# Optimization experiments

Measured on AMD Instinct MI355X. Metric: run time of the kernel, lower is better.

Reference implementation:

```python
import jax, jax.numpy as jnp
import numpy as np

H = 256        # hidden_size
MAX_LEN = 200  # position table has MAX_LEN+1 rows
B = 4096       # number of sessions


def setup_inputs() -> dict:
    rng = np.random.RandomState(0)
    # ragged session lengths in [10, 100)
    seq_len = rng.randint(10, 100, size=B).astype(np.int64)
    T = int(seq_len.sum())
    # reverse positions: len-1, ..., 1, 0 per session (as the torch code uses)
    reverse_pos = np.concatenate([np.arange(l - 1, -1, -1) for l in seq_len]).astype(np.int64)

    key = jax.random.key(0)
    ks = jax.random.split(key, 8)
    def lin(k, fin, fout):
        # torch Linear init ~ U(-1/sqrt(fin), 1/sqrt(fin)); store as [fin, fout]
        lim = 1.0 / np.sqrt(fin)
        kw, kb = jax.random.split(k)
        W = jax.random.uniform(kw, (fin, fout), jnp.float32, -lim, lim)
        b = jax.random.uniform(kb, (fout,), jnp.float32, -lim, lim)
        return W, b

    hidden = jax.random.normal(ks[0], (T, H), jnp.float32)
    pos_table = jax.random.normal(ks[1], (MAX_LEN + 1, H), jnp.float32)
    W_pos, b_pos = lin(ks[2], 2 * H, H)   # W_pos_inter
    W1, b1 = lin(ks[3], H, H)             # W_1_inter
    W2, b2 = lin(ks[4], H, H)             # W_2_inter
    qw, qb = lin(ks[5], H, 1)             # q_inter

    return {
        "hidden": hidden,
        "pos_table": pos_table,
        "W_pos": W_pos, "b_pos": b_pos,
        "W1": W1, "b1": b1,
        "W2": W2, "b2": b2,
        "qw": qw, "qb": qb,
        "seq_len": jnp.asarray(seq_len),
        "reverse_pos": jnp.asarray(reverse_pos),
    }


def reference(hidden, pos_table, W_pos, b_pos, W1, b1, W2, b2, qw, qb, seq_len, reverse_pos):
    T = hidden.shape[0]
    nb = seq_len.shape[0]
    # segment id per token (sessions are contiguous)
    seg = jnp.repeat(jnp.arange(nb), seq_len, total_repeat_length=T)  # [T]
    # per-session mean, gathered back per token (v_mean_repeat_concat)
    sess_mean = jax.ops.segment_sum(hidden, seg, num_segments=nb)
    sess_mean = sess_mean / seq_len[:, None].astype(hidden.dtype)
    v_mean = sess_mean[seg]                                           # [T, H]
    # position-augmented hidden: tanh(W_pos_inter([hidden; pos_emb]))
    pos_emb = pos_table[reverse_pos]                                  # [T, H]
    pos_hidden = jnp.tanh(jnp.concatenate([hidden, pos_emb], -1) @ W_pos + b_pos)
    # alpha = q_inter(sigmoid(W_1_inter(v_mean) + W_2_inter(pos_hidden)))
    gate = jax.nn.sigmoid(v_mean @ W1 + b1 + pos_hidden @ W2 + b2)
    alpha = gate @ qw + qb                                            # [T, 1]
    # per-session weighted sum of hidden
    h_s = jax.ops.segment_sum(alpha * hidden, seg, num_segments=nb)   # [B, H]
    return h_s
```

## Files before the change

kernel.cpp:

```cpp
#include <hip/hip_runtime.h>
#include <hip/hip_bf16.h>
#include <stdint.h>

#define HD 256
#define BM 64
#define BK 32
#define PAD 8

typedef __bf16 bf16x8 __attribute__((ext_vector_type(8)));
typedef float f32x4 __attribute__((ext_vector_type(4)));
typedef unsigned short ushort8 __attribute__((ext_vector_type(8)));

__device__ __forceinline__ unsigned short f2bf(float f) {
    unsigned int x = __float_as_uint(f);
    unsigned int r = (x + 0x7FFFu + ((x >> 16) & 1u)) >> 16;
    return (unsigned short)r;
}

__global__ void scan_kernel(const int* __restrict__ seq_len, int* __restrict__ offsets, int B) {
    __shared__ int sums[256];
    int tid = threadIdx.x;
    int per = (B + 255) / 256;
    int b0 = tid * per;
    int local[32];
    int tot = 0;
    for (int i = 0; i < per && i < 32; ++i) {
        int b = b0 + i;
        int v = (b < B) ? seq_len[b] : 0;
        local[i] = tot;
        tot += v;
    }
    sums[tid] = tot;
    __syncthreads();
    for (int off = 1; off < 256; off <<= 1) {
        int v = (tid >= off) ? sums[tid - off] : 0;
        __syncthreads();
        sums[tid] += v;
        __syncthreads();
    }
    int start = sums[tid] - tot;
    for (int i = 0; i < per && i < 32; ++i) {
        int b = b0 + i;
        if (b < B) offsets[b] = start + local[i];
    }
    if (tid == 255) offsets[B] = sums[255];
}

__global__ void seg_kernel(const int* __restrict__ offsets, int* __restrict__ seg) {
    int b = blockIdx.x;
    int s = offsets[b], e = offsets[b + 1];
    for (int t = s + threadIdx.x; t < e; t += blockDim.x) seg[t] = b;
}

__global__ void mean_kernel(const float* __restrict__ hidden, const int* __restrict__ offsets,
                            float* __restrict__ mean) {
    int b = blockIdx.x;
    int s = offsets[b], e = offsets[b + 1];
    int tid = threadIdx.x;
    int g = tid >> 6, c = tid & 63;
    float4 acc = {0.f, 0.f, 0.f, 0.f};
    for (int t = s + g; t < e; t += 4) {
        const float4 v = *reinterpret_cast<const float4*>(hidden + (size_t)t * HD + c * 4);
        acc.x += v.x; acc.y += v.y; acc.z += v.z; acc.w += v.w;
    }
    __shared__ float4 part[4][64];
    part[g][c] = acc;
    __syncthreads();
    if (g == 0) {
        float4 a0 = part[0][c], a1 = part[1][c], a2 = part[2][c], a3 = part[3][c];
        float inv = 1.0f / (float)(e - s);
        float4 m;
        m.x = (a0.x + a1.x + a2.x + a3.x) * inv;
        m.y = (a0.y + a1.y + a2.y + a3.y) * inv;
        m.z = (a0.z + a1.z + a2.z + a3.z) * inv;
        m.w = (a0.w + a1.w + a2.w + a3.w) * inv;
        *reinterpret_cast<float4*>(mean + (size_t)b * HD + c * 4) = m;
    }
}

__global__ void transpose_kernel(const float* __restrict__ Wp, const float* __restrict__ W1,
                                 const float* __restrict__ W2,
                                 unsigned short* __restrict__ WphT, unsigned short* __restrict__ WpbT,
                                 unsigned short* __restrict__ W1T, unsigned short* __restrict__ W2T) {
    int n = blockIdx.x;
    int k = threadIdx.x;
    WphT[n * HD + k] = f2bf(Wp[k * HD + n]);
    WpbT[n * HD + k] = f2bf(Wp[(HD + k) * HD + n]);
    W1T[n * HD + k]  = f2bf(W1[k * HD + n]);
    W2T[n * HD + k]  = f2bf(W2[k * HD + n]);
}

__global__ __launch_bounds__(256) void gemm_bias_kernel(
    const float* __restrict__ A, int M,
    const unsigned short* __restrict__ BT,
    const float* __restrict__ bias1, const float* __restrict__ bias2,
    float* __restrict__ out) {
    __shared__ __align__(16) unsigned short As[BM][BK + PAD];
    __shared__ __align__(16) unsigned short Bs[HD][BK + PAD];
    int tid = threadIdx.x;
    int m0 = blockIdx.x * BM;
    int wave = tid >> 6, lane = tid & 63, quad = lane >> 4, cc = lane & 15;
    int nb = wave * 64;
    f32x4 acc[4][4];
    for (int i = 0; i < 4; ++i) for (int j = 0; j < 4; ++j) acc[i][j] = (f32x4){0.f, 0.f, 0.f, 0.f};
    int arow = tid >> 2, acg = (tid & 3) * 8;

    for (int kc = 0; kc < HD; kc += BK) {
        {
            int m = m0 + arow;
            float4 f0 = {0,0,0,0}, f1 = {0,0,0,0};
            if (m < M) {
                const float4* p = reinterpret_cast<const float4*>(A + (size_t)m * HD + kc + acg);
                f0 = p[0]; f1 = p[1];
            }
            ushort8 pk;
            pk[0] = f2bf(f0.x); pk[1] = f2bf(f0.y); pk[2] = f2bf(f0.z); pk[3] = f2bf(f0.w);
            pk[4] = f2bf(f1.x); pk[5] = f2bf(f1.y); pk[6] = f2bf(f1.z); pk[7] = f2bf(f1.w);
            *reinterpret_cast<ushort8*>(&As[arow][acg]) = pk;
        }
        for (int i = 0; i < 4; ++i) {
            int n = i * 64 + (tid >> 2);
            int c8 = (tid & 3) * 8;
            ushort8 v = *reinterpret_cast<const ushort8*>(BT + (size_t)n * HD + kc + c8);
            *reinterpret_cast<ushort8*>(&Bs[n][c8]) = v;
        }
        __syncthreads();
        bf16x8 af[4], bfr[4];
        for (int mf = 0; mf < 4; ++mf) af[mf] = *reinterpret_cast<const bf16x8*>(&As[mf * 16 + cc][quad * 8]);
        for (int nf = 0; nf < 4; ++nf) bfr[nf] = *reinterpret_cast<const bf16x8*>(&Bs[nb + nf * 16 + cc][quad * 8]);
        for (int mf = 0; mf < 4; ++mf)
            for (int nf = 0; nf < 4; ++nf)
                acc[mf][nf] = __builtin_amdgcn_mfma_f32_16x16x32_bf16(af[mf], bfr[nf], acc[mf][nf], 0, 0, 0);
        __syncthreads();
    }
    for (int mf = 0; mf < 4; ++mf)
        for (int nf = 0; nf < 4; ++nf)
            for (int r = 0; r < 4; ++r) {
                int row = m0 + mf * 16 + quad * 4 + r;
                int col = nb + nf * 16 + cc;
                if (row < M) {
                    float v = acc[mf][nf][r] + bias1[col];
                    if (bias2) v += bias2[col];
                    out[(size_t)row * HD + col] = v;
                }
            }
}

__global__ __launch_bounds__(256) void main_kernel(
    const float* __restrict__ hidden, int T,
    const unsigned short* __restrict__ WphT,
    const unsigned short* __restrict__ W2T,
    const float* __restrict__ P2,
    const float* __restrict__ u,
    const float* __restrict__ qw, const float* __restrict__ qb,
    const int* __restrict__ rp, const int* __restrict__ seg,
    float* __restrict__ alpha) {
    __shared__ __align__(16) unsigned short As[BM][BK + PAD];
    __shared__ __align__(16) unsigned short Bs[HD][BK + PAD];
    __shared__ __align__(16) unsigned short Ph[BM][HD + PAD];
    __shared__ int rp_s[BM];
    __shared__ int seg_s[BM];
    __shared__ float alpha_s[BM];

    int tid = threadIdx.x;
    int t0 = blockIdx.x * BM;
    if (tid < BM) {
        int t = t0 + tid;
        rp_s[tid]  = (t < T) ? rp[t] : 0;
        seg_s[tid] = (t < T) ? seg[t] : 0;
        alpha_s[tid] = qb[0];
    }
    int wave = tid >> 6, lane = tid & 63, quad = lane >> 4, cc = lane & 15;
    int nb = wave * 64;
    f32x4 acc[4][4];
    for (int i = 0; i < 4; ++i) for (int j = 0; j < 4; ++j) acc[i][j] = (f32x4){0.f, 0.f, 0.f, 0.f};
    int arow = tid >> 2, acg = (tid & 3) * 8;

    for (int kc = 0; kc < HD; kc += BK) {
        {
            int t = t0 + arow;
            float4 f0 = {0,0,0,0}, f1 = {0,0,0,0};
            if (t < T) {
                const float4* p = reinterpret_cast<const float4*>(hidden + (size_t)t * HD + kc + acg);
                f0 = p[0]; f1 = p[1];
            }
            ushort8 pk;
            pk[0] = f2bf(f0.x); pk[1] = f2bf(f0.y); pk[2] = f2bf(f0.z); pk[3] = f2bf(f0.w);
            pk[4] = f2bf(f1.x); pk[5] = f2bf(f1.y); pk[6] = f2bf(f1.z); pk[7] = f2bf(f1.w);
            *reinterpret_cast<ushort8*>(&As[arow][acg]) = pk;
        }
        for (int i = 0; i < 4; ++i) {
            int n = i * 64 + (tid >> 2);
            int c8 = (tid & 3) * 8;
            ushort8 v = *reinterpret_cast<const ushort8*>(WphT + (size_t)n * HD + kc + c8);
            *reinterpret_cast<ushort8*>(&Bs[n][c8]) = v;
        }
        __syncthreads();
        bf16x8 af[4], bfr[4];
        for (int mf = 0; mf < 4; ++mf) af[mf] = *reinterpret_cast<const bf16x8*>(&As[mf * 16 + cc][quad * 8]);
        for (int nf = 0; nf < 4; ++nf) bfr[nf] = *reinterpret_cast<const bf16x8*>(&Bs[nb + nf * 16 + cc][quad * 8]);
        for (int mf = 0; mf < 4; ++mf)
            for (int nf = 0; nf < 4; ++nf)
                acc[mf][nf] = __builtin_amdgcn_mfma_f32_16x16x32_bf16(af[mf], bfr[nf], acc[mf][nf], 0, 0, 0);
        __syncthreads();
    }

    for (int mf = 0; mf < 4; ++mf)
        for (int nf = 0; nf < 4; ++nf)
            for (int r = 0; r < 4; ++r) {
                int row = mf * 16 + quad * 4 + r;
                int col = nb + nf * 16 + cc;
                float v = acc[mf][nf][r] + P2[(size_t)rp_s[row] * HD + col];
                Ph[row][col] = f2bf(tanhf(v));
                acc[mf][nf][r] = 0.f;
            }
    __syncthreads();

    for (int kc = 0; kc < HD; kc += BK) {
        for (int i = 0; i < 4; ++i) {
            int n = i * 64 + (tid >> 2);
            int c8 = (tid & 3) * 8;
            ushort8 v = *reinterpret_cast<const ushort8*>(W2T + (size_t)n * HD + kc + c8);
            *reinterpret_cast<ushort8*>(&Bs[n][c8]) = v;
        }
        __syncthreads();
        bf16x8 af[4], bfr[4];
        for (int mf = 0; mf < 4; ++mf) af[mf] = *reinterpret_cast<const bf16x8*>(&Ph[mf * 16 + cc][kc + quad * 8]);
        for (int nf = 0; nf < 4; ++nf) bfr[nf] = *reinterpret_cast<const bf16x8*>(&Bs[nb + nf * 16 + cc][quad * 8]);
        for (int mf = 0; mf < 4; ++mf)
            for (int nf = 0; nf < 4; ++nf)
                acc[mf][nf] = __builtin_amdgcn_mfma_f32_16x16x32_bf16(af[mf], bfr[nf], acc[mf][nf], 0, 0, 0);
        __syncthreads();
    }

    float qwv[4];
    for (int nf = 0; nf < 4; ++nf) qwv[nf] = qw[nb + nf * 16 + cc];
    for (int mf = 0; mf < 4; ++mf)
        for (int r = 0; r < 4; ++r) {
            int row = mf * 16 + quad * 4 + r;
            const float* urow = u + (size_t)seg_s[row] * HD;
            float s = 0.f;
            for (int nf = 0; nf < 4; ++nf) {
                float g = acc[mf][nf][r] + urow[nb + nf * 16 + cc];
                g = 1.0f / (1.0f + __expf(-g));
                s += g * qwv[nf];
            }
            s += __shfl_xor(s, 1);
            s += __shfl_xor(s, 2);
            s += __shfl_xor(s, 4);
            s += __shfl_xor(s, 8);
            if (cc == 0) atomicAdd(&alpha_s[row], s);
        }
    __syncthreads();
    if (tid < BM) {
        int t = t0 + tid;
        if (t < T) alpha[t] = alpha_s[tid];
    }
}

__global__ void hs_kernel(const float* __restrict__ hidden, const float* __restrict__ alpha,
                          const int* __restrict__ offsets, float* __restrict__ out) {
    int b = blockIdx.x;
    int s = offsets[b], e = offsets[b + 1];
    int tid = threadIdx.x;
    __shared__ float al[256];
    for (int i = tid; i < e - s; i += 256) al[i] = alpha[s + i];
    __syncthreads();
    int g = tid >> 6, c = tid & 63;
    float4 acc = {0.f, 0.f, 0.f, 0.f};
    for (int t = s + g; t < e; t += 4) {
        float a = al[t - s];
        const float4 v = *reinterpret_cast<const float4*>(hidden + (size_t)t * HD + c * 4);
        acc.x += a * v.x; acc.y += a * v.y; acc.z += a * v.z; acc.w += a * v.w;
    }
    __shared__ float4 part[4][64];
    part[g][c] = acc;
    __syncthreads();
    if (g == 0) {
        float4 a0 = part[0][c], a1 = part[1][c], a2 = part[2][c], a3 = part[3][c];
        float4 m;
        m.x = a0.x + a1.x + a2.x + a3.x;
        m.y = a0.y + a1.y + a2.y + a3.y;
        m.z = a0.z + a1.z + a2.z + a3.z;
        m.w = a0.w + a1.w + a2.w + a3.w;
        *reinterpret_cast<float4*>(out + (size_t)b * HD + c * 4) = m;
    }
}

extern "C" void kernel_launch(void* const* d_in, const int* in_sizes, int n_in,
                              void* d_out, int out_size, void* d_ws, size_t ws_size,
                              hipStream_t stream) {
    (void)n_in; (void)out_size; (void)ws_size;
    const float* hidden    = (const float*)d_in[0];
    const float* pos_table = (const float*)d_in[1];
    const float* W_pos     = (const float*)d_in[2];
    const float* b_pos     = (const float*)d_in[3];
    const float* W1        = (const float*)d_in[4];
    const float* b1        = (const float*)d_in[5];
    const float* W2        = (const float*)d_in[6];
    const float* b2        = (const float*)d_in[7];
    const float* qw        = (const float*)d_in[8];
    const float* qb        = (const float*)d_in[9];
    const int* seq_len     = (const int*)d_in[10];
    const int* reverse_pos = (const int*)d_in[11];

    int T  = in_sizes[0] / HD;
    int B  = in_sizes[10];
    int NP = in_sizes[1] / HD;

    char* ws = (char*)d_ws;
    auto carve = [&](size_t bytes) -> char* {
        char* p = ws;
        ws += (bytes + 255) & ~(size_t)255;
        return p;
    };
    int* offsets         = (int*)carve((size_t)(B + 1) * sizeof(int));
    int* seg             = (int*)carve((size_t)T * sizeof(int));
    float* mean          = (float*)carve((size_t)B * HD * sizeof(float));
    float* u             = (float*)carve((size_t)B * HD * sizeof(float));
    float* P2            = (float*)carve((size_t)NP * HD * sizeof(float));
    unsigned short* WphT = (unsigned short*)carve((size_t)HD * HD * 2);
    unsigned short* WpbT = (unsigned short*)carve((size_t)HD * HD * 2);
    unsigned short* W1T  = (unsigned short*)carve((size_t)HD * HD * 2);
    unsigned short* W2T  = (unsigned short*)carve((size_t)HD * HD * 2);
    float* alpha         = (float*)carve((size_t)T * sizeof(float));

    scan_kernel<<<1, 256, 0, stream>>>(seq_len, offsets, B);
    seg_kernel<<<B, 64, 0, stream>>>(offsets, seg);
    mean_kernel<<<B, 256, 0, stream>>>(hidden, offsets, mean);
    transpose_kernel<<<HD, HD, 0, stream>>>(W_pos, W1, W2, WphT, WpbT, W1T, W2T);
    gemm_bias_kernel<<<(NP + BM - 1) / BM, 256, 0, stream>>>(pos_table, NP, WpbT, b_pos, nullptr, P2);
    gemm_bias_kernel<<<(B + BM - 1) / BM, 256, 0, stream>>>(mean, B, W1T, b1, b2, u);
    main_kernel<<<(T + BM - 1) / BM, 256, 0, stream>>>(hidden, T, WphT, W2T, P2, u, qw, qb,
                                                       reverse_pos, seg, alpha);
    hs_kernel<<<B, 256, 0, stream>>>(hidden, alpha, offsets, (float*)d_out);
}
```

Measured before the change: 654.1 us.

## Stage full A tile in LDS once, read weights from global, fuse seg into mean

The GEMM kernels now load the entire 64x256 activation tile into LDS once, converted to bf16. Weight fragments are read directly from global memory (L2-resident) instead of being staged through LDS each K step, which removes the per-iteration barriers. The first GEMM in main_kernel is transposed (weights as A, tokens as B) so the tanh epilogue can write vectorized bf16 results back into the same LDS buffer, and tanhf is replaced by an exp-based formula. The seg fill is folded into mean_kernel to drop one launch, and __launch_bounds__(256,4) asks for higher occupancy, at the risk of more global weight traffic and register pressure.

```diff
diff --git a/kernel.cpp b/kernel.cpp
--- a/kernel.cpp
+++ b/kernel.cpp
@@ -5,11 +5,13 @@
 #define HD 256
 #define BM 64
 #define BK 32
-#define PAD 8
+#define APAD 8
+#define ASTRIDE (HD + APAD)
 
 typedef __bf16 bf16x8 __attribute__((ext_vector_type(8)));
 typedef float f32x4 __attribute__((ext_vector_type(4)));
-typedef unsigned short ushort8 __attribute__((ext_vector_type(8)));
+typedef unsigned short ushort8v __attribute__((ext_vector_type(8)));
+typedef unsigned short us4 __attribute__((ext_vector_type(4)));
 
 __device__ __forceinline__ unsigned short f2bf(float f) {
     unsigned int x = __float_as_uint(f);
@@ -46,17 +48,12 @@
     if (tid == 255) offsets[B] = sums[255];
 }
 
-__global__ void seg_kernel(const int* __restrict__ offsets, int* __restrict__ seg) {
+__global__ void mean_kernel(const float* __restrict__ hidden, const int* __restrict__ offsets,
+                            float* __restrict__ mean, int* __restrict__ seg) {
     int b = blockIdx.x;
     int s = offsets[b], e = offsets[b + 1];
-    for (int t = s + threadIdx.x; t < e; t += blockDim.x) seg[t] = b;
-}
-
-__global__ void mean_kernel(const float* __restrict__ hidden, const int* __restrict__ offsets,
-                            float* __restrict__ mean) {
-    int b = blockIdx.x;
-    int s = offsets[b], e = offsets[b + 1];
-    int tid = threadIdx.x;
+    int tid = threadIdx.x;
+    for (int t = s + tid; t < e; t += 256) seg[t] = b;
     int g = tid >> 6, c = tid & 63;
     float4 acc = {0.f, 0.f, 0.f, 0.f};
     for (int t = s + g; t < e; t += 4) {
@@ -95,43 +92,41 @@
     const unsigned short* __restrict__ BT,
     const float* __restrict__ bias1, const float* __restrict__ bias2,
     float* __restrict__ out) {
-    __shared__ __align__(16) unsigned short As[BM][BK + PAD];
-    __shared__ __align__(16) unsigned short Bs[HD][BK + PAD];
+    __shared__ __align__(16) unsigned short As[BM][ASTRIDE];
     int tid = threadIdx.x;
     int m0 = blockIdx.x * BM;
     int wave = tid >> 6, lane = tid & 63, quad = lane >> 4, cc = lane & 15;
     int nb = wave * 64;
     f32x4 acc[4][4];
     for (int i = 0; i < 4; ++i) for (int j = 0; j < 4; ++j) acc[i][j] = (f32x4){0.f, 0.f, 0.f, 0.f};
-    int arow = tid >> 2, acg = (tid & 3) * 8;
-
-    for (int kc = 0; kc < HD; kc += BK) {
-        {
-            int m = m0 + arow;
+
+    {
+        int row = tid >> 2;
+        int m = m0 + row;
+        for (int i = 0; i < 8; ++i) {
+            int cg = ((tid & 3) + 4 * i) * 8;
             float4 f0 = {0,0,0,0}, f1 = {0,0,0,0};
             if (m < M) {
-                const float4* p = reinterpret_cast<const float4*>(A + (size_t)m * HD + kc + acg);
+                const float4* p = reinterpret_cast<const float4*>(A + (size_t)m * HD + cg);
                 f0 = p[0]; f1 = p[1];
             }
-            ushort8 pk;
+            ushort8v pk;
             pk[0] = f2bf(f0.x); pk[1] = f2bf(f0.y); pk[2] = f2bf(f0.z); pk[3] = f2bf(f0.w);
             pk[4] = f2bf(f1.x); pk[5] = f2bf(f1.y); pk[6] = f2bf(f1.z); pk[7] = f2bf(f1.w);
-            *reinterpret_cast<ushort8*>(&As[arow][acg]) = pk;
-        }
-        for (int i = 0; i < 4; ++i) {
-            int n = i * 64 + (tid >> 2);
-            int c8 = (tid & 3) * 8;
-            ushort8 v = *reinterpret_cast<const ushort8*>(BT + (size_t)n * HD + kc + c8);
-            *reinterpret_cast<ushort8*>(&Bs[n][c8]) = v;
-        }
-        __syncthreads();
-        bf16x8 af[4], bfr[4];
-        for (int mf = 0; mf < 4; ++mf) af[mf] = *reinterpret_cast<const bf16x8*>(&As[mf * 16 + cc][quad * 8]);
-        for (int nf = 0; nf < 4; ++nf) bfr[nf] = *reinterpret_cast<const bf16x8*>(&Bs[nb + nf * 16 + cc][quad * 8]);
-        for (int mf = 0; mf < 4; ++mf)
+            *reinterpret_cast<ushort8v*>(&As[row][cg]) = pk;
+        }
+    }
+    __syncthreads();
+
+    for (int kc = 0; kc < HD; kc += BK) {
+        bf16x8 bfr[4];
+        for (int nf = 0; nf < 4; ++nf)
+            bfr[nf] = *reinterpret_cast<const bf16x8*>(BT + (size_t)(nb + nf * 16 + cc) * HD + kc + quad * 8);
+        for (int mf = 0; mf < 4; ++mf) {
+            bf16x8 af = *reinterpret_cast<const bf16x8*>(&As[mf * 16 + cc][kc + quad * 8]);
             for (int nf = 0; nf < 4; ++nf)
-                acc[mf][nf] = __builtin_amdgcn_mfma_f32_16x16x32_bf16(af[mf], bfr[nf], acc[mf][nf], 0, 0, 0);
-        __syncthreads();
+                acc[mf][nf] = __builtin_amdgcn_mfma_f32_16x16x32_bf16(af, bfr[nf], acc[mf][nf], 0, 0, 0);
+        }
     }
     for (int mf = 0; mf < 4; ++mf)
         for (int nf = 0; nf < 4; ++nf)
@@ -146,7 +141,7 @@
             }
 }
 
-__global__ __launch_bounds__(256) void main_kernel(
+__global__ __launch_bounds__(256, 4) void main_kernel(
     const float* __restrict__ hidden, int T,
     const unsigned short* __restrict__ WphT,
     const unsigned short* __restrict__ W2T,
@@ -155,93 +150,98 @@
     const float* __restrict__ qw, const float* __restrict__ qb,
     const int* __restrict__ rp, const int* __restrict__ seg,
     float* __restrict__ alpha) {
-    __shared__ __align__(16) unsigned short As[BM][BK + PAD];
-    __shared__ __align__(16) unsigned short Bs[HD][BK + PAD];
-    __shared__ __align__(16) unsigned short Ph[BM][HD + PAD];
+    __shared__ __align__(16) unsigned short Ah[BM][ASTRIDE];
     __shared__ int rp_s[BM];
     __shared__ int seg_s[BM];
     __shared__ float alpha_s[BM];
 
     int tid = threadIdx.x;
     int t0 = blockIdx.x * BM;
+    int wave = tid >> 6, lane = tid & 63, quad = lane >> 4, cc = lane & 15;
+    int mb = wave * 64;
+
+    {
+        int row = tid >> 2;
+        int t = t0 + row;
+        for (int i = 0; i < 8; ++i) {
+            int cg = ((tid & 3) + 4 * i) * 8;
+            float4 f0 = {0,0,0,0}, f1 = {0,0,0,0};
+            if (t < T) {
+                const float4* p = reinterpret_cast<const float4*>(hidden + (size_t)t * HD + cg);
+                f0 = p[0]; f1 = p[1];
+            }
+            ushort8v pk;
+            pk[0] = f2bf(f0.x); pk[1] = f2bf(f0.y); pk[2] = f2bf(f0.z); pk[3] = f2bf(f0.w);
+            pk[4] = f2bf(f1.x); pk[5] = f2bf(f1.y); pk[6] = f2bf(f1.z); pk[7] = f2bf(f1.w);
+            *reinterpret_cast<ushort8v*>(&Ah[row][cg]) = pk;
+        }
+    }
     if (tid < BM) {
         int t = t0 + tid;
         rp_s[tid]  = (t < T) ? rp[t] : 0;
         seg_s[tid] = (t < T) ? seg[t] : 0;
         alpha_s[tid] = qb[0];
     }
-    int wave = tid >> 6, lane = tid & 63, quad = lane >> 4, cc = lane & 15;
-    int nb = wave * 64;
+    __syncthreads();
+
     f32x4 acc[4][4];
     for (int i = 0; i < 4; ++i) for (int j = 0; j < 4; ++j) acc[i][j] = (f32x4){0.f, 0.f, 0.f, 0.f};
-    int arow = tid >> 2, acg = (tid & 3) * 8;
 
     for (int kc = 0; kc < HD; kc += BK) {
-        {
-            int t = t0 + arow;
-            float4 f0 = {0,0,0,0}, f1 = {0,0,0,0};
-            if (t < T) {
-                const float4* p = reinterpret_cast<const float4*>(hidden + (size_t)t * HD + kc + acg);
-                f0 = p[0]; f1 = p[1];
-            }
-            ushort8 pk;
-            pk[0] = f2bf(f0.x); pk[1] = f2bf(f0.y); pk[2] = f2bf(f0.z); pk[3] = f2bf(f0.w);
-            pk[4] = f2bf(f1.x); pk[5] = f2bf(f1.y); pk[6] = f2bf(f1.z); pk[7] = f2bf(f1.w);
-            *reinterpret_cast<ushort8*>(&As[arow][acg]) = pk;
-        }
-        for (int i = 0; i < 4; ++i) {
-            int n = i * 64 + (tid >> 2);
-            int c8 = (tid & 3) * 8;
-            ushort8 v = *reinterpret_cast<const ushort8*>(WphT + (size_t)n * HD + kc + c8);
-            *reinterpret_cast<ushort8*>(&Bs[n][c8]) = v;
-        }
-        __syncthreads();
-        bf16x8 af[4], bfr[4];
-        for (int mf = 0; mf < 4; ++mf) af[mf] = *reinterpret_cast<const bf16x8*>(&As[mf * 16 + cc][quad * 8]);
-        for (int nf = 0; nf < 4; ++nf) bfr[nf] = *reinterpret_cast<const bf16x8*>(&Bs[nb + nf * 16 + cc][quad * 8]);
-        for (int mf = 0; mf < 4; ++mf)
+        bf16x8 bfr[4];
+        for (int nf = 0; nf < 4; ++nf)
+            bfr[nf] = *reinterpret_cast<const bf16x8*>(&Ah[nf * 16 + cc][kc + quad * 8]);
+        for (int mf = 0; mf < 4; ++mf) {
+            bf16x8 af = *reinterpret_cast<const bf16x8*>(WphT + (size_t)(mb + mf * 16 + cc) * HD + kc + quad * 8);
             for (int nf = 0; nf < 4; ++nf)
-                acc[mf][nf] = __builtin_amdgcn_mfma_f32_16x16x32_bf16(af[mf], bfr[nf], acc[mf][nf], 0, 0, 0);
-        __syncthreads();
-    }
+                acc[mf][nf] = __builtin_amdgcn_mfma_f32_16x16x32_bf16(af, bfr[nf], acc[mf][nf], 0, 0, 0);
+        }
+    }
+    __syncthreads();
 
     for (int mf = 0; mf < 4; ++mf)
+        for (int nf = 0; nf < 4; ++nf) {
+            int token = nf * 16 + cc;
+            int h0 = mb + mf * 16 + quad * 4;
+            const float4 p2v = *reinterpret_cast<const float4*>(P2 + (size_t)rp_s[token] * HD + h0);
+            us4 pk;
+            {
+                float v0 = acc[mf][nf][0] + p2v.x;
+                float v1 = acc[mf][nf][1] + p2v.y;
+                float v2 = acc[mf][nf][2] + p2v.z;
+                float v3 = acc[mf][nf][3] + p2v.w;
+                float e0 = __expf(2.f * v0), e1 = __expf(2.f * v1);
+                float e2 = __expf(2.f * v2), e3 = __expf(2.f * v3);
+                pk[0] = f2bf(1.f - 2.f / (e0 + 1.f));
+                pk[1] = f2bf(1.f - 2.f / (e1 + 1.f));
+                pk[2] = f2bf(1.f - 2.f / (e2 + 1.f));
+                pk[3] = f2bf(1.f - 2.f / (e3 + 1.f));
+            }
+            *reinterpret_cast<us4*>(&Ah[token][h0]) = pk;
+            acc[mf][nf] = (f32x4){0.f, 0.f, 0.f, 0.f};
+        }
+    __syncthreads();
+
+    for (int kc = 0; kc < HD; kc += BK) {
+        bf16x8 bfr[4];
         for (int nf = 0; nf < 4; ++nf)
-            for (int r = 0; r < 4; ++r) {
-                int row = mf * 16 + quad * 4 + r;
-                int col = nb + nf * 16 + cc;
-                float v = acc[mf][nf][r] + P2[(size_t)rp_s[row] * HD + col];
-                Ph[row][col] = f2bf(tanhf(v));
-                acc[mf][nf][r] = 0.f;
-            }
-    __syncthreads();
-
-    for (int kc = 0; kc < HD; kc += BK) {
-        for (int i = 0; i < 4; ++i) {
-            int n = i * 64 + (tid >> 2);
-            int c8 = (tid & 3) * 8;
-            ushort8 v = *reinterpret_cast<const ushort8*>(W2T + (size_t)n * HD + kc + c8);
-            *reinterpret_cast<ushort8*>(&Bs[n][c8]) = v;
-        }
-        __syncthreads();
-        bf16x8 af[4], bfr[4];
-        for (int mf = 0; mf < 4; ++mf) af[mf] = *reinterpret_cast<const bf16x8*>(&Ph[mf * 16 + cc][kc + quad * 8]);
-        for (int nf = 0; nf < 4; ++nf) bfr[nf] = *reinterpret_cast<const bf16x8*>(&Bs[nb + nf * 16 + cc][quad * 8]);
-        for (int mf = 0; mf < 4; ++mf)
+            bfr[nf] = *reinterpret_cast<const bf16x8*>(W2T + (size_t)(mb + nf * 16 + cc) * HD + kc + quad * 8);
+        for (int mf = 0; mf < 4; ++mf) {
+            bf16x8 af = *reinterpret_cast<const bf16x8*>(&Ah[mf * 16 + cc][kc + quad * 8]);
             for (int nf = 0; nf < 4; ++nf)
-                acc[mf][nf] = __builtin_amdgcn_mfma_f32_16x16x32_bf16(af[mf], bfr[nf], acc[mf][nf], 0, 0, 0);
-        __syncthreads();
+                acc[mf][nf] = __builtin_amdgcn_mfma_f32_16x16x32_bf16(af, bfr[nf], acc[mf][nf], 0, 0, 0);
+        }
     }
 
     float qwv[4];
-    for (int nf = 0; nf < 4; ++nf) qwv[nf] = qw[nb + nf * 16 + cc];
+    for (int nf = 0; nf < 4; ++nf) qwv[nf] = qw[mb + nf * 16 + cc];
     for (int mf = 0; mf < 4; ++mf)
         for (int r = 0; r < 4; ++r) {
-            int row = mf * 16 + quad * 4 + r;
-            const float* urow = u + (size_t)seg_s[row] * HD;
+            int token = mf * 16 + quad * 4 + r;
+            const float* urow = u + (size_t)seg_s[token] * HD;
             float s = 0.f;
             for (int nf = 0; nf < 4; ++nf) {
-                float g = acc[mf][nf][r] + urow[nb + nf * 16 + cc];
+                float g = acc[mf][nf][r] + urow[mb + nf * 16 + cc];
                 g = 1.0f / (1.0f + __expf(-g));
                 s += g * qwv[nf];
             }
@@ -249,7 +249,7 @@
             s += __shfl_xor(s, 2);
             s += __shfl_xor(s, 4);
             s += __shfl_xor(s, 8);
-            if (cc == 0) atomicAdd(&alpha_s[row], s);
+            if (cc == 0) atomicAdd(&alpha_s[token], s);
         }
     __syncthreads();
     if (tid < BM) {
@@ -326,9 +326,8 @@
     float* alpha         = (float*)carve((size_t)T * sizeof(float));
 
     scan_kernel<<<1, 256, 0, stream>>>(seq_len, offsets, B);
-    seg_kernel<<<B, 64, 0, stream>>>(offsets, seg);
-    mean_kernel<<<B, 256, 0, stream>>>(hidden, offsets, mean);
     transpose_kernel<<<HD, HD, 0, stream>>>(W_pos, W1, W2, WphT, WpbT, W1T, W2T);
+    mean_kernel<<<B, 256, 0, stream>>>(hidden, offsets, mean, seg);
     gemm_bias_kernel<<<(NP + BM - 1) / BM, 256, 0, stream>>>(pos_table, NP, WpbT, b_pos, nullptr, P2);
     gemm_bias_kernel<<<(B + BM - 1) / BM, 256, 0, stream>>>(mean, B, W1T, b1, b2, u);
     main_kernel<<<(T + BM - 1) / BM, 256, 0, stream>>>(hidden, T, WphT, W2T, P2, u, qw, qb,
```

Result: faster. 594.2 us (-9.2%).
